# Performance work log

Measured on AMD Instinct MI355X. Metric: run time of the kernel, lower is better.

The kernel has to match this reference:

```python
import jax, jax.numpy as jnp
import numpy as np

D = 768
HEAD_SIZE = 64  # D / num_heads = 768 / 12

def setup_inputs() -> dict:
    key = jax.random.key(0)
    k1, k2, k3, k4 = jax.random.split(key, 4)
    ix = jax.random.normal(k1, (8, 4096, D), dtype=jnp.float32)
    # Linear(D, head_size, bias=False) weights; stored as [D, head_size] for x @ W
    scale = 1.0 / np.sqrt(D)
    Wk = jax.random.uniform(k2, (D, HEAD_SIZE), dtype=jnp.float32, minval=-scale, maxval=scale)
    Wq = jax.random.uniform(k3, (D, HEAD_SIZE), dtype=jnp.float32, minval=-scale, maxval=scale)
    Wv = jax.random.uniform(k4, (D, HEAD_SIZE), dtype=jnp.float32, minval=-scale, maxval=scale)
    return {"ix": ix, "Wk": Wk, "Wq": Wq, "Wv": Wv}

def reference(ix, Wk, Wq, Wv):
    # ix: [B, S, D]
    k = ix @ Wk  # [B, S, H]
    q = ix @ Wq  # [B, S, H]
    v = ix @ Wv  # [B, S, H]
    scale = 1.0 / jnp.sqrt(jnp.asarray(HEAD_SIZE, ix.dtype))
    wei = jnp.einsum('bsh,bth->bst', q, k) * scale  # [B, S, S]
    wei = jax.nn.softmax(wei, axis=-1)
    out = jnp.einsum('bst,bth->bsh', wei, v)  # [B, S, H]
    return out
```

## Files before the change

kernel.cpp:

```cpp
#include <hip/hip_runtime.h>
#include <hip/hip_bf16.h>

#define D_DIM 768
#define HS 64
#define SEQ 4096
#define NBATCH 8

typedef short bf8 __attribute__((ext_vector_type(8)));
typedef short bf4 __attribute__((ext_vector_type(4)));
typedef float f4 __attribute__((ext_vector_type(4)));

static __device__ __forceinline__ short f2b(float x) {
    __hip_bfloat16 h = __float2bfloat16(x);
    return __builtin_bit_cast(short, h);
}
static __device__ __forceinline__ unsigned pk2(float x, float y) {
    unsigned ux = __builtin_bit_cast(unsigned, x) + 0x8000u;
    unsigned uy = __builtin_bit_cast(unsigned, y) + 0x8000u;
    return __builtin_amdgcn_perm(uy, ux, 0x07060302u);
}

#if defined(__has_builtin)
#if __has_builtin(__builtin_amdgcn_exp2f)
#define EXP2F(x) __builtin_amdgcn_exp2f(x)
#endif
#endif
#ifndef EXP2F
#define EXP2F(x) exp2f(x)
#endif

__global__ __launch_bounds__(256) void wconv_kernel(
    const float* __restrict__ Wk, const float* __restrict__ Wq,
    const float* __restrict__ Wv, short* __restrict__ wt3)
{
    int tid = blockIdx.x * 256 + threadIdx.x;
    int mat = tid / (D_DIM * HS);
    int rem = tid - mat * (D_DIM * HS);
    int k = rem >> 6;
    int n = rem & 63;
    const float* W = (mat == 0) ? Wk : (mat == 1) ? Wq : Wv;
    float scale = (mat == 1) ? 0.18033688011112042f : 1.0f;
    int cc = mat * HS + n;
    int c = k >> 5, q = (k >> 3) & 3, e = k & 7;
    wt3[(c * 192 + cc) * 32 + q * 8 + e] = f2b(W[rem] * scale);
}

__global__ __launch_bounds__(256, 3) void proj_kernel(
    const float* __restrict__ ix, const short* __restrict__ wt3,
    short* __restrict__ qg, short* __restrict__ kg, short* __restrict__ vg)
{
    __shared__ short ixl[2][32 * 72];

    const int t = threadIdx.x;
    const int wave = t >> 6, lane = t & 63;
    const int m = lane & 15, quad = lane >> 4;
    const int m0 = blockIdx.x * 32;

    const int srow = t >> 3;
    const int skoff = (t & 7) * 8;

    f4 xr0, xr1;
    auto load_ix = [&](int c) {
        const float* px = ix + (m0 + srow) * D_DIM + c * 64 + skoff;
        xr0 = *(const f4*)px;
        xr1 = *(const f4*)(px + 4);
    };
    auto write_ix = [&](int p) {
        bf8 xw;
        #pragma unroll
        for (int i = 0; i < 4; ++i) { xw[i] = f2b(xr0[i]); xw[i + 4] = f2b(xr1[i]); }
        *(bf8*)(&ixl[p][srow * 72 + skoff]) = xw;
    };

    const int colb = wave * 48;
    const short* wbase = wt3 + (colb + m) * 32 + quad * 8;

    bf8 wb[2][2][3];
    auto load_w = [&](int c, int buf) {
        #pragma unroll
        for (int nt = 0; nt < 3; ++nt) {
            const short* pw = wbase + ((size_t)(2 * c) * 192 + nt * 16) * 32;
            wb[buf][0][nt] = *(const bf8*)pw;
            wb[buf][1][nt] = *(const bf8*)(pw + 192 * 32);
        }
    };

    f4 acc[2][3] = {};

    load_ix(0); load_w(0, 0); write_ix(0); __syncthreads();

    #pragma unroll
    for (int c = 0; c < 12; ++c) {
        const int p = c & 1;
        if (c + 1 < 12) { load_ix(c + 1); load_w(c + 1, (c + 1) & 1); }

        bf8 a0 = *(const bf8*)(&ixl[p][m * 72 + quad * 8]);
        bf8 a1 = *(const bf8*)(&ixl[p][m * 72 + 32 + quad * 8]);
        bf8 a2 = *(const bf8*)(&ixl[p][(16 + m) * 72 + quad * 8]);
        bf8 a3 = *(const bf8*)(&ixl[p][(16 + m) * 72 + 32 + quad * 8]);

        #pragma unroll
        for (int nt = 0; nt < 3; ++nt) {
            acc[0][nt] = __builtin_amdgcn_mfma_f32_16x16x32_bf16(a0, wb[p][0][nt], acc[0][nt], 0, 0, 0);
            acc[0][nt] = __builtin_amdgcn_mfma_f32_16x16x32_bf16(a1, wb[p][1][nt], acc[0][nt], 0, 0, 0);
            acc[1][nt] = __builtin_amdgcn_mfma_f32_16x16x32_bf16(a2, wb[p][0][nt], acc[1][nt], 0, 0, 0);
            acc[1][nt] = __builtin_amdgcn_mfma_f32_16x16x32_bf16(a3, wb[p][1][nt], acc[1][nt], 0, 0, 0);
        }

        if (c + 1 < 12) { write_ix((c + 1) & 1); __syncthreads(); }
    }

    #pragma unroll
    for (int mt = 0; mt < 2; ++mt) {
        const int row = m0 + mt * 16 + quad * 4;
        #pragma unroll
        for (int nt = 0; nt < 3; ++nt) {
            const int cb = colb + nt * 16;
            short* op = (cb < 64) ? kg : (cb < 128) ? qg : vg;
            const int n = (cb & 63) + m;
            #pragma unroll
            for (int r = 0; r < 4; ++r)
                op[(row + r) * HS + n] = f2b(acc[mt][nt][r]);
        }
    }
}

__global__ __launch_bounds__(256, 2) void attn_kernel(
    const short* __restrict__ qg, const short* __restrict__ kg,
    const short* __restrict__ vg, float* __restrict__ num0,
    float* __restrict__ num1, float* __restrict__ num2,
    float* __restrict__ num3, float* __restrict__ den0,
    float* __restrict__ den1, float* __restrict__ den2,
    float* __restrict__ den3)
{
    __shared__ short kl[2][64 * 72];
    __shared__ short vl[2][64 * 64];

    const int t = threadIdx.x;
    const int wave = t >> 6, lane = t & 63;
    const int m = lane & 15, quad = lane >> 4;

    const int flat = blockIdx.x;
    const int lg = (flat & 7) * 64 + (flat >> 3);
    const int qx = lg & 15;
    const int ks = (lg >> 4) & 3;
    const int b  = lg >> 6;

    const int rbase = b * SEQ;
    const int kbase = rbase + ks * (SEQ / 4);
    const int qw = qx * 256 + wave * 64;

    float* __restrict__ nump = (ks == 0) ? num0 : (ks == 1) ? num1 : (ks == 2) ? num2 : num3;
    float* __restrict__ denp = (ks == 0) ? den0 : (ks == 1) ? den1 : (ks == 2) ? den2 : den3;

    bf8 qf[4][2];
    #pragma unroll
    for (int nq = 0; nq < 4; ++nq)
        #pragma unroll
        for (int st = 0; st < 2; ++st)
            qf[nq][st] = *(const bf8*)(qg + (rbase + qw + nq * 16 + m) * HS + st * 32 + quad * 8);

    const int srow = t >> 2, soff = (t & 3) * 16;
    const int jp = t >> 3, dg = t & 7;
    const int j0 = jp * 2;
    const int jj = j0 & 31;
    const int gj = j0 >> 5;
    const int vq = (jj >> 2) & 3;
    const int vh = (jj >> 4) & 1;
    const int vb = (jj & 3) >> 1;
    const int vcol_base = vh * 4 + 2 * vb;
    const int vchunk_l = 4 * gj + vq;

    uint4 kr0, kr1, vr0, vr1;
    auto load_chunk = [&](int c) {
        const short* pk = kg + (kbase + c * 64 + srow) * HS + soff;
        kr0 = *(const uint4*)pk; kr1 = *(const uint4*)(pk + 8);
        const short* pv = vg + (kbase + c * 64 + j0) * HS + dg * 8;
        vr0 = *(const uint4*)pv; vr1 = *(const uint4*)(pv + HS);
    };
    auto write_chunk = [&](int p) {
        *(bf8*)(&kl[p][srow * 72 + soff])     = __builtin_bit_cast(bf8, kr0);
        *(bf8*)(&kl[p][srow * 72 + soff + 8]) = __builtin_bit_cast(bf8, kr1);
        bf8 v0 = __builtin_bit_cast(bf8, vr0), v1 = __builtin_bit_cast(bf8, vr1);
        #pragma unroll
        for (int i = 0; i < 8; ++i) {
            const int d = dg * 8 + i;
            const int chunk = vchunk_l ^ (i ^ dg);
            unsigned val = (unsigned short)v0[i] | ((unsigned)(unsigned short)v1[i] << 16);
            *(unsigned*)(&vl[p][d * 64 + chunk * 8 + vcol_base]) = val;
        }
    };

    f4 o[4][4] = {};
    float den[4] = {0.f, 0.f, 0.f, 0.f};

    load_chunk(0); write_chunk(0); __syncthreads();

    const int NCH = SEQ / 4 / 64;
    for (int c = 0; c < NCH; ++c) {
        const int p = c & 1;
        if (c + 1 < NCH) load_chunk(c + 1);

        #pragma unroll
        for (int g = 0; g < 2; ++g) {
            bf8 kA0 = *(const bf8*)(&kl[p][(g * 32 + m) * 72 + quad * 8]);
            bf8 kA1 = *(const bf8*)(&kl[p][(g * 32 + m) * 72 + 32 + quad * 8]);
            bf8 kB0 = *(const bf8*)(&kl[p][(g * 32 + 16 + m) * 72 + quad * 8]);
            bf8 kB1 = *(const bf8*)(&kl[p][(g * 32 + 16 + m) * 72 + 32 + quad * 8]);

            bf8 vf[4];
            #pragma unroll
            for (int dt = 0; dt < 4; ++dt) {
                const int row = dt * 16 + m;
                const int key = (m & 7) ^ (2 * dt + (m >> 3));
                const int chunk = (g * 4 + quad) ^ key;
                vf[dt] = *(const bf8*)(&vl[p][row * 64 + chunk * 8]);
            }

            #pragma unroll
            for (int nq = 0; nq < 4; ++nq) {
                f4 sa = {0.f, 0.f, 0.f, 0.f}, sb = {0.f, 0.f, 0.f, 0.f};
                sa = __builtin_amdgcn_mfma_f32_16x16x32_bf16(kA0, qf[nq][0], sa, 0, 0, 0);
                sa = __builtin_amdgcn_mfma_f32_16x16x32_bf16(kA1, qf[nq][1], sa, 0, 0, 0);
                sb = __builtin_amdgcn_mfma_f32_16x16x32_bf16(kB0, qf[nq][0], sb, 0, 0, 0);
                sb = __builtin_amdgcn_mfma_f32_16x16x32_bf16(kB1, qf[nq][1], sb, 0, 0, 0);
                float e0 = EXP2F(sa[0]), e1 = EXP2F(sa[1]), e2 = EXP2F(sa[2]), e3 = EXP2F(sa[3]);
                float e4 = EXP2F(sb[0]), e5 = EXP2F(sb[1]), e6 = EXP2F(sb[2]), e7 = EXP2F(sb[3]);
                den[nq] += ((e0 + e1) + (e2 + e3)) + ((e4 + e5) + (e6 + e7));
                uint4 pu;
                pu.x = pk2(e0, e1); pu.y = pk2(e2, e3);
                pu.z = pk2(e4, e5); pu.w = pk2(e6, e7);
                bf8 pf = __builtin_bit_cast(bf8, pu);
                #pragma unroll
                for (int dt = 0; dt < 4; ++dt)
                    o[nq][dt] = __builtin_amdgcn_mfma_f32_16x16x32_bf16(vf[dt], pf, o[nq][dt], 0, 0, 0);
            }
        }

        if (c + 1 < NCH) { write_chunk((c + 1) & 1); __syncthreads(); }
    }

    #pragma unroll
    for (int nq = 0; nq < 4; ++nq) {
        float d = den[nq];
        d += __shfl_xor(d, 16, 64);
        d += __shfl_xor(d, 32, 64);
        const int orow = rbase + qw + nq * 16 + m;
        if (quad == 0) denp[orow] = d;
        #pragma unroll
        for (int dt = 0; dt < 4; ++dt)
            *(f4*)(nump + orow * HS + dt * 16 + quad * 4) = o[nq][dt];
    }
}

__global__ __launch_bounds__(256) void reduce_kernel(
    float* __restrict__ out, const float* __restrict__ num1,
    const float* __restrict__ num2, const float* __restrict__ num3,
    const float* __restrict__ den0, const float* __restrict__ den1,
    const float* __restrict__ den2, const float* __restrict__ den3)
{
    const int gid = blockIdx.x * 256 + threadIdx.x;
    const int base = gid * 4;
    const int r = base >> 6;
    f4 n0 = *(const f4*)(out + base);
    f4 n1 = *(const f4*)(num1 + base);
    f4 n2 = *(const f4*)(num2 + base);
    f4 n3 = *(const f4*)(num3 + base);
    const float rs = 1.0f / ((den0[r] + den1[r]) + (den2[r] + den3[r]));
    f4 res;
    #pragma unroll
    for (int i = 0; i < 4; ++i) res[i] = ((n0[i] + n1[i]) + (n2[i] + n3[i])) * rs;
    *(f4*)(out + base) = res;
}

extern "C" void kernel_launch(void* const* d_in, const int* in_sizes, int n_in,
                              void* d_out, int out_size, void* d_ws, size_t ws_size,
                              hipStream_t stream) {
    const float* ix = (const float*)d_in[0];
    const float* Wk = (const float*)d_in[1];
    const float* Wq = (const float*)d_in[2];
    const float* Wv = (const float*)d_in[3];
    float* out = (float*)d_out;

    const size_t NQKV = (size_t)NBATCH * SEQ * HS;
    short* qg = (short*)d_ws;
    short* kg = qg + NQKV;
    short* vg = kg + NQKV;
    short* wt3 = vg + NQKV;
    char*  fbase = (char*)(wt3 + 24 * 192 * 32);
    float* num1 = (float*)fbase;
    float* num2 = num1 + NQKV;
    float* num3 = num2 + NQKV;
    float* den0 = num3 + NQKV;
    float* den1 = den0 + (size_t)NBATCH * SEQ;
    float* den2 = den1 + (size_t)NBATCH * SEQ;
    float* den3 = den2 + (size_t)NBATCH * SEQ;

    wconv_kernel<<<(3 * D_DIM * HS) / 256, 256, 0, stream>>>(Wk, Wq, Wv, wt3);
    proj_kernel<<<(NBATCH * SEQ) / 32, 256, 0, stream>>>(ix, wt3, qg, kg, vg);
    attn_kernel<<<512, 256, 0, stream>>>(qg, kg, vg, out, num1, num2, num3,
                                         den0, den1, den2, den3);
    reduce_kernel<<<(int)(NQKV / (256 * 4)), 256, 0, stream>>>(
        out, num1, num2, num3, den0, den1, den2, den3);
}
```

Before: 216.4 us.

## Split attention keys eight ways, raise occupancy, and deepen projection prefetch

The attention kernel now splits each batch's keys into eight partitions instead of four, doubling the grid to 1024 blocks with per-split numerator and denominator buffers. Occupancy is raised to four blocks per SM, and wave priority is set around the MFMA section. The projection kernel is reworked to prefetch input chunks two steps ahead using two register sets, and packs bf16 with the round-by-add helper. The intent is to fill more compute units and hide load latency, at the cost of more partial-sum traffic in the reduce step and extra register pressure.

Measured after the change: 659.4 us. +204.8%, slower.

```diff
diff --git a/kernel.cpp b/kernel.cpp
--- a/kernel.cpp
+++ b/kernel.cpp
@@ -59,17 +59,19 @@
     const int srow = t >> 3;
     const int skoff = (t & 7) * 8;
 
-    f4 xr0, xr1;
-    auto load_ix = [&](int c) {
+    f4 xa0, xa1, xb0, xb1;
+    auto load_ix = [&](int c, f4& r0, f4& r1) {
         const float* px = ix + (m0 + srow) * D_DIM + c * 64 + skoff;
-        xr0 = *(const f4*)px;
-        xr1 = *(const f4*)(px + 4);
-    };
-    auto write_ix = [&](int p) {
-        bf8 xw;
-        #pragma unroll
-        for (int i = 0; i < 4; ++i) { xw[i] = f2b(xr0[i]); xw[i + 4] = f2b(xr1[i]); }
-        *(bf8*)(&ixl[p][srow * 72 + skoff]) = xw;
+        r0 = *(const f4*)px;
+        r1 = *(const f4*)(px + 4);
+    };
+    auto write_ix = [&](int p, f4 r0, f4 r1) {
+        uint4 xw;
+        xw.x = pk2(r0[0], r0[1]);
+        xw.y = pk2(r0[2], r0[3]);
+        xw.z = pk2(r1[0], r1[1]);
+        xw.w = pk2(r1[2], r1[3]);
+        *(uint4*)(&ixl[p][srow * 72 + skoff]) = xw;
     };
 
     const int colb = wave * 48;
@@ -87,18 +89,18 @@
 
     f4 acc[2][3] = {};
 
-    load_ix(0); load_w(0, 0); write_ix(0); __syncthreads();
-
-    #pragma unroll
-    for (int c = 0; c < 12; ++c) {
-        const int p = c & 1;
-        if (c + 1 < 12) { load_ix(c + 1); load_w(c + 1, (c + 1) & 1); }
-
+    load_ix(0, xa0, xa1);
+    load_w(0, 0);
+    write_ix(0, xa0, xa1);
+    load_ix(1, xb0, xb1);
+    load_w(1, 1);
+    __syncthreads();
+
+    auto mfma_block = [&](int p) {
         bf8 a0 = *(const bf8*)(&ixl[p][m * 72 + quad * 8]);
         bf8 a1 = *(const bf8*)(&ixl[p][m * 72 + 32 + quad * 8]);
         bf8 a2 = *(const bf8*)(&ixl[p][(16 + m) * 72 + quad * 8]);
         bf8 a3 = *(const bf8*)(&ixl[p][(16 + m) * 72 + 32 + quad * 8]);
-
         #pragma unroll
         for (int nt = 0; nt < 3; ++nt) {
             acc[0][nt] = __builtin_amdgcn_mfma_f32_16x16x32_bf16(a0, wb[p][0][nt], acc[0][nt], 0, 0, 0);
@@ -106,8 +108,23 @@
             acc[1][nt] = __builtin_amdgcn_mfma_f32_16x16x32_bf16(a2, wb[p][0][nt], acc[1][nt], 0, 0, 0);
             acc[1][nt] = __builtin_amdgcn_mfma_f32_16x16x32_bf16(a3, wb[p][1][nt], acc[1][nt], 0, 0, 0);
         }
-
-        if (c + 1 < 12) { write_ix((c + 1) & 1); __syncthreads(); }
+    };
+
+    for (int cc = 0; cc < 12; cc += 2) {
+        {
+            const int c = cc;
+            if (c + 2 < 12) load_ix(c + 2, xa0, xa1);
+            mfma_block(0);
+            if (c + 2 < 12) load_w(c + 2, 0);
+            if (c + 1 < 12) { write_ix(1, xb0, xb1); __syncthreads(); }
+        }
+        {
+            const int c = cc + 1;
+            if (c + 2 < 12) load_ix(c + 2, xb0, xb1);
+            mfma_block(1);
+            if (c + 2 < 12) load_w(c + 2, 1);
+            if (c + 1 < 12) { write_ix(0, xa0, xa1); __syncthreads(); }
+        }
     }
 
     #pragma unroll
@@ -125,13 +142,17 @@
     }
 }
 
-__global__ __launch_bounds__(256, 2) void attn_kernel(
+__global__ __launch_bounds__(256, 4) void attn_kernel(
     const short* __restrict__ qg, const short* __restrict__ kg,
-    const short* __restrict__ vg, float* __restrict__ num0,
-    float* __restrict__ num1, float* __restrict__ num2,
-    float* __restrict__ num3, float* __restrict__ den0,
-    float* __restrict__ den1, float* __restrict__ den2,
-    float* __restrict__ den3)
+    const short* __restrict__ vg,
+    float* __restrict__ num0, float* __restrict__ num1,
+    float* __restrict__ num2, float* __restrict__ num3,
+    float* __restrict__ num4, float* __restrict__ num5,
+    float* __restrict__ num6, float* __restrict__ num7,
+    float* __restrict__ den0, float* __restrict__ den1,
+    float* __restrict__ den2, float* __restrict__ den3,
+    float* __restrict__ den4, float* __restrict__ den5,
+    float* __restrict__ den6, float* __restrict__ den7)
 {
     __shared__ short kl[2][64 * 72];
     __shared__ short vl[2][64 * 64];
@@ -141,17 +162,21 @@
     const int m = lane & 15, quad = lane >> 4;
 
     const int flat = blockIdx.x;
-    const int lg = (flat & 7) * 64 + (flat >> 3);
+    const int lg = (flat & 7) * 128 + (flat >> 3);
     const int qx = lg & 15;
-    const int ks = (lg >> 4) & 3;
-    const int b  = lg >> 6;
+    const int ks = (lg >> 4) & 7;
+    const int b  = lg >> 7;
 
     const int rbase = b * SEQ;
-    const int kbase = rbase + ks * (SEQ / 4);
+    const int kbase = rbase + ks * (SEQ / 8);
     const int qw = qx * 256 + wave * 64;
 
-    float* __restrict__ nump = (ks == 0) ? num0 : (ks == 1) ? num1 : (ks == 2) ? num2 : num3;
-    float* __restrict__ denp = (ks == 0) ? den0 : (ks == 1) ? den1 : (ks == 2) ? den2 : den3;
+    float* __restrict__ nump =
+        (ks == 0) ? num0 : (ks == 1) ? num1 : (ks == 2) ? num2 : (ks == 3) ? num3 :
+        (ks == 4) ? num4 : (ks == 5) ? num5 : (ks == 6) ? num6 : num7;
+    float* __restrict__ denp =
+        (ks == 0) ? den0 : (ks == 1) ? den1 : (ks == 2) ? den2 : (ks == 3) ? den3 :
+        (ks == 4) ? den4 : (ks == 5) ? den5 : (ks == 6) ? den6 : den7;
 
     bf8 qf[4][2];
     #pragma unroll
@@ -196,11 +221,12 @@
 
     load_chunk(0); write_chunk(0); __syncthreads();
 
-    const int NCH = SEQ / 4 / 64;
+    const int NCH = SEQ / 8 / 64;
     for (int c = 0; c < NCH; ++c) {
         const int p = c & 1;
         if (c + 1 < NCH) load_chunk(c + 1);
 
+        __builtin_amdgcn_s_setprio(1);
         #pragma unroll
         for (int g = 0; g < 2; ++g) {
             bf8 kA0 = *(const bf8*)(&kl[p][(g * 32 + m) * 72 + quad * 8]);
@@ -236,6 +262,7 @@
                     o[nq][dt] = __builtin_amdgcn_mfma_f32_16x16x32_bf16(vf[dt], pf, o[nq][dt], 0, 0, 0);
             }
         }
+        __builtin_amdgcn_s_setprio(0);
 
         if (c + 1 < NCH) { write_chunk((c + 1) & 1); __syncthreads(); }
     }
@@ -256,8 +283,12 @@
 __global__ __launch_bounds__(256) void reduce_kernel(
     float* __restrict__ out, const float* __restrict__ num1,
     const float* __restrict__ num2, const float* __restrict__ num3,
+    const float* __restrict__ num4, const float* __restrict__ num5,
+    const float* __restrict__ num6, const float* __restrict__ num7,
     const float* __restrict__ den0, const float* __restrict__ den1,
-    const float* __restrict__ den2, const float* __restrict__ den3)
+    const float* __restrict__ den2, const float* __restrict__ den3,
+    const float* __restrict__ den4, const float* __restrict__ den5,
+    const float* __restrict__ den6, const float* __restrict__ den7)
 {
     const int gid = blockIdx.x * 256 + threadIdx.x;
     const int base = gid * 4;
@@ -266,10 +297,17 @@
     f4 n1 = *(const f4*)(num1 + base);
     f4 n2 = *(const f4*)(num2 + base);
     f4 n3 = *(const f4*)(num3 + base);
-    const float rs = 1.0f / ((den0[r] + den1[r]) + (den2[r] + den3[r]));
+    f4 n4 = *(const f4*)(num4 + base);
+    f4 n5 = *(const f4*)(num5 + base);
+    f4 n6 = *(const f4*)(num6 + base);
+    f4 n7 = *(const f4*)(num7 + base);
+    const float dsum = ((den0[r] + den1[r]) + (den2[r] + den3[r]))
+                     + ((den4[r] + den5[r]) + (den6[r] + den7[r]));
+    const float rs = 1.0f / dsum;
     f4 res;
     #pragma unroll
-    for (int i = 0; i < 4; ++i) res[i] = ((n0[i] + n1[i]) + (n2[i] + n3[i])) * rs;
+    for (int i = 0; i < 4; ++i)
+        res[i] = (((n0[i] + n1[i]) + (n2[i] + n3[i])) + ((n4[i] + n5[i]) + (n6[i] + n7[i]))) * rs;
     *(f4*)(out + base) = res;
 }
 
@@ -283,6 +321,7 @@
     float* out = (float*)d_out;
 
     const size_t NQKV = (size_t)NBATCH * SEQ * HS;
+    const size_t NR = (size_t)NBATCH * SEQ;
     short* qg = (short*)d_ws;
     short* kg = qg + NQKV;
     short* vg = kg + NQKV;
@@ -291,15 +330,25 @@
     float* num1 = (float*)fbase;
     float* num2 = num1 + NQKV;
     float* num3 = num2 + NQKV;
-    float* den0 = num3 + NQKV;
-    float* den1 = den0 + (size_t)NBATCH * SEQ;
-    float* den2 = den1 + (size_t)NBATCH * SEQ;
-    float* den3 = den2 + (size_t)NBATCH * SEQ;
+    float* num4 = num3 + NQKV;
+    float* num5 = num4 + NQKV;
+    float* num6 = num5 + NQKV;
+    float* num7 = num6 + NQKV;
+    float* den0 = num7 + NQKV;
+    float* den1 = den0 + NR;
+    float* den2 = den1 + NR;
+    float* den3 = den2 + NR;
+    float* den4 = den3 + NR;
+    float* den5 = den4 + NR;
+    float* den6 = den5 + NR;
+    float* den7 = den6 + NR;
 
     wconv_kernel<<<(3 * D_DIM * HS) / 256, 256, 0, stream>>>(Wk, Wq, Wv, wt3);
     proj_kernel<<<(NBATCH * SEQ) / 32, 256, 0, stream>>>(ix, wt3, qg, kg, vg);
-    attn_kernel<<<512, 256, 0, stream>>>(qg, kg, vg, out, num1, num2, num3,
-                                         den0, den1, den2, den3);
+    attn_kernel<<<1024, 256, 0, stream>>>(qg, kg, vg,
+                                          out, num1, num2, num3, num4, num5, num6, num7,
+                                          den0, den1, den2, den3, den4, den5, den6, den7);
     reduce_kernel<<<(int)(NQKV / (256 * 4)), 256, 0, stream>>>(
-        out, num1, num2, num3, den0, den1, den2, den3);
-}
+        out, num1, num2, num3, num4, num5, num6, num7,
+        den0, den1, den2, den3, den4, den5, den6, den7);
+}
```
